# Performance work log

Hardware: AMD Instinct MI355X
Metric: run time of the kernel (lower is better)

## Reference

```python
import jax, jax.numpy as jnp
import numpy as np

H = 256  # hidden_size
B = 8192  # batch
S = 1024  # seq_length


def setup_inputs() -> dict:
    key = jax.random.key(0)
    ks = jax.random.split(key, 12)
    lim_g = 1.0 / np.sqrt(1 + H)  # torch Linear default init bound, fan_in = 1+H
    lim_o = 1.0 / np.sqrt(H)
    def lin(k, out_dim, in_dim, lim):
        kw, kb = jax.random.split(k)
        W = jax.random.uniform(kw, (out_dim, in_dim), jnp.float32, -lim, lim)
        b = jax.random.uniform(kb, (out_dim,), jnp.float32, -lim, lim)
        return W, b
    Wf, bf = lin(ks[0], H, 1 + H, lim_g)
    Wi, bi = lin(ks[1], H, 1 + H, lim_g)
    Wc, bc = lin(ks[2], H, 1 + H, lim_g)
    Wo, bo = lin(ks[3], H, 1 + H, lim_g)
    Wout, bout = lin(ks[4], 1, H, lim_o)
    x = jax.random.normal(ks[5], (B, S), jnp.float32)
    return {"x": x, "Wf": Wf, "bf": bf, "Wi": Wi, "bi": bi,
            "Wc": Wc, "bc": bc, "Wo": Wo, "bo": bo,
            "Wout": Wout, "bout": bout}


def reference(x, Wf, bf, Wi, bi, Wc, bc, Wo, bo, Wout, bout):
    B_, S_ = x.shape
    H_ = Wf.shape[0]
    # Fuse the four gate linears into one GEMM per step (same math):
    Wall = jnp.concatenate([Wf, Wi, Wc, Wo], axis=0)      # [4H, 1+H]
    ball = jnp.concatenate([bf, bi, bc, bo], axis=0)      # [4H]

    def step(carry, xt):
        h, c = carry                                       # [B,H], [B,H]
        conc = jnp.concatenate([xt[:, None], h], axis=1)   # [B, 1+H]
        g = conc @ Wall.T + ball                           # [B, 4H]
        f, i, cs, o = jnp.split(g, 4, axis=1)
        c = jax.nn.sigmoid(f) * c + jax.nn.sigmoid(i) * jnp.tanh(cs)
        h = jax.nn.sigmoid(o) * jnp.tanh(c)
        return (h, c), None

    h0 = jnp.zeros((B_, H_), x.dtype)
    c0 = jnp.zeros((B_, H_), x.dtype)
    (h, _), _ = jax.lax.scan(step, (h0, c0), x.T)          # scan over seq axis
    out = h @ Wout.T + bout                                # [B, 1]
    return out.squeeze(-1)                                 # [B]
```

## Files before the change

### kernel.cpp

```cpp
#include <hip/hip_runtime.h>
#include <hip/hip_fp16.h>


typedef _Float16 f16x8 __attribute__((ext_vector_type(8)));
typedef float f32x4 __attribute__((ext_vector_type(4)));
typedef unsigned int u32;
typedef unsigned short u16;

#define WINT_OFF 0u
#define W0B_OFF  524288u
#define FLAG_OFF 528384u
#define PUB_OFF  1048576u

static __device__ __forceinline__ float fast_exp2(float x) {
#if __has_builtin(__builtin_amdgcn_exp2f)
  return __builtin_amdgcn_exp2f(x);
#else
  return exp2f(x);
#endif
}
static __device__ __forceinline__ float fast_rcp(float x) {
#if __has_builtin(__builtin_amdgcn_rcpf)
  return __builtin_amdgcn_rcpf(x);
#else
  return 1.0f / x;
#endif
}
static __device__ __forceinline__ u16 f16b(float f) {
  union { _Float16 h; u16 u; } cv; cv.h = (_Float16)f; return cv.u;
}
static __device__ __forceinline__ float h2f(u16 u) {
  union { u16 u; _Float16 h; } cv; cv.u = u; return (float)cv.h;
}
static __device__ __forceinline__ u16* pub_base(u16* pub, int set, int par,
                                                int pid, int half) {
  return pub + ((size_t)(((set * 2 + par) * 128 + pid) * 2 + half) << 12);
}

__global__ void lstm_prep(const float* __restrict__ Wf, const float* __restrict__ Wi,
                          const float* __restrict__ Wc, const float* __restrict__ Wo,
                          const float* __restrict__ bf_, const float* __restrict__ bi_,
                          const float* __restrict__ bc_, const float* __restrict__ bo_,
                          u16* __restrict__ Wint, u32* __restrict__ w0b) {
  int n = blockIdx.x;
  int k = threadIdx.x;
  int g = n >> 8, j = n & 255;
  const float* Ws = (g == 0) ? Wf : (g == 1) ? Wi : (g == 2) ? Wc : Wo;
  const float scale = (g == 2) ? 2.88539008f : 1.44269504f;
  Wint[n * 256 + k] = f16b(Ws[j * 257 + 1 + k] * scale);
  if (k == 0) {
    const float* bs = (g == 0) ? bf_ : (g == 1) ? bi_ : (g == 2) ? bc_ : bo_;
    w0b[n] = (u32)f16b(Ws[j * 257] * scale) | ((u32)f16b(bs[j] * scale) << 16);
  }
}

__global__ void lstm_zero(uint4* __restrict__ pub4, uint4* __restrict__ flags4,
                          float* __restrict__ out, const float* __restrict__ bout) {
  int idx = blockIdx.x * 256 + threadIdx.x;
  uint4 z = uint4{0, 0, 0, 0};
  if (idx < 131072) pub4[idx] = z;
  else if (idx < 262144) pub4[idx + 131072] = z;
  else if (idx < 264192) flags4[idx - 262144] = z;
  else { int o = idx - 264192; if (o < 8192) out[o] = bout[0]; }
}

__global__ __launch_bounds__(512, 2) void lstm_main(
    const u16* __restrict__ Wint, const u32* __restrict__ w0b,
    const float* __restrict__ x, const float* __restrict__ Wout,
    float* __restrict__ out, u16* __restrict__ pub, int* __restrict__ flags) {

  __shared__ __align__(16) u16 stg[2][2][4096];

  const int tid  = threadIdx.x;
  const int wv   = tid >> 6;
  const int lane = tid & 63;
  const int l15  = lane & 15;
  const int quad = lane >> 4;
  const int B    = blockIdx.x;
  const int mi   = (B >> 3) & 1;
  const int peer = B ^ 8;
  const int pid  = (B & 7) | ((B >> 4) << 3);
  const int rows0 = pid * 64;

  f16x8 wfrag[4][8];
#pragma unroll
  for (int g = 0; g < 4; ++g)
#pragma unroll
    for (int hm = 0; hm < 2; ++hm)
#pragma unroll
      for (int ktl = 0; ktl < 4; ++ktl) {
        int kbase = (hm == 0 ? mi : 1 - mi) * 128 + ktl * 32;
        wfrag[g][hm * 4 + ktl] = *(const f16x8*)(Wint +
            (size_t)(g * 256 + mi * 128 + wv * 16 + l15) * 256 + kbase + quad * 8);
      }
  float w0f[4][4], bsf[4][4];
#pragma unroll
  for (int g = 0; g < 4; ++g) {
    uint4 wv4 = *(const uint4*)(w0b + g * 256 + mi * 128 + wv * 16 + quad * 4);
    u32 pka[4] = {wv4.x, wv4.y, wv4.z, wv4.w};
#pragma unroll
    for (int r = 0; r < 4; ++r) {
      w0f[g][r] = h2f((u16)pka[r]);
      bsf[g][r] = h2f((u16)(pka[r] >> 16));
    }
  }

#pragma unroll
  for (int i = 0; i < 4; ++i) ((uint4*)stg)[tid + i * 512] = uint4{0, 0, 0, 0};

  float cst[2][2][4];
#pragma unroll
  for (int s = 0; s < 2; ++s)
#pragma unroll
    for (int bt = 0; bt < 2; ++bt)
#pragma unroll
      for (int r = 0; r < 4; ++r) cst[s][bt][r] = 0.0f;

  const float* xq = x + (size_t)rows0 * 1024;
  float xcur[2][2];
#pragma unroll
  for (int s = 0; s < 2; ++s)
#pragma unroll
    for (int bt = 0; bt < 2; ++bt)
      xcur[s][bt] = xq[(size_t)(s * 32 + bt * 16 + l15) * 1024];

  int* const myflag = flags + B * 32;
  int* const pfl    = flags + peer * 32;

  __syncthreads();

#pragma unroll 1
  for (int t = 0; t < 1024; ++t) {
#pragma unroll
    for (int s = 0; s < 2; ++s) {
      f32x4 acc[4][2];
#pragma unroll
      for (int g = 0; g < 4; ++g)
#pragma unroll
        for (int r = 0; r < 4; ++r) {
          acc[g][0][r] = xcur[s][0] * w0f[g][r] + bsf[g][r];
          acc[g][1][r] = xcur[s][1] * w0f[g][r] + bsf[g][r];
        }
#pragma unroll
      for (int bt = 0; bt < 2; ++bt)
        xcur[s][bt] = xq[(size_t)(s * 32 + bt * 16 + l15) * 1024 + ((t + 1) & 1023)];

#pragma unroll
      for (int hm = 0; hm < 2; ++hm)
#pragma unroll
        for (int ktl = 0; ktl < 4; ++ktl) {
          f16x8 bb[2];
#pragma unroll
          for (int bt = 0; bt < 2; ++bt) {
            int b = bt * 16 + l15;
            int cp = (ktl * 4 + quad) ^ (b & 15);
            bb[bt] = *(const f16x8*)(&stg[s][hm][0] + b * 128 + cp * 8);
          }
#pragma unroll
          for (int g = 0; g < 4; ++g)
#pragma unroll
            for (int bt = 0; bt < 2; ++bt)
              acc[g][bt] = __builtin_amdgcn_mfma_f32_16x16x32_f16(
                  wfrag[g][hm * 4 + ktl], bb[bt], acc[g][bt], 0, 0, 0);
        }

      const int tn = (s == 0) ? t : t + 1;
      if (tn < 1024) {
        while (__hip_atomic_load(pfl + (s ^ 1) * 16, __ATOMIC_RELAXED,
                                 __HIP_MEMORY_SCOPE_AGENT) < tn)
          __builtin_amdgcn_s_sleep(1);
        const u16* srcO = pub_base(pub, s ^ 1, tn & 1, pid, mi);
        const u16* srcP = pub_base(pub, s ^ 1, tn & 1, pid, 1 - mi);
        __builtin_amdgcn_global_load_lds(
            (const __attribute__((address_space(1))) u32*)(srcO + wv * 512 + lane * 8),
            (__attribute__((address_space(3))) u32*)(&stg[s ^ 1][0][wv * 512]), 16, 0, 0);
        __builtin_amdgcn_global_load_lds(
            (const __attribute__((address_space(1))) u32*)(srcP + wv * 512 + lane * 8),
            (__attribute__((address_space(3))) u32*)(&stg[s ^ 1][1][wv * 512]), 16, 0, 0);
      }

      u16* pb = pub_base(pub, s, (t + 1) & 1, pid, mi);
#pragma unroll
      for (int bt = 0; bt < 2; ++bt) {
        int b = bt * 16 + l15;
        u32 lo, hi;
        {
          float h0, h1, h2, h3;
#pragma unroll
          for (int r = 0; r < 4; ++r) {
            float fg = acc[0][bt][r], ig = acc[1][bt][r];
            float cg = acc[2][bt][r], og = acc[3][bt][r];
            float Ef = fast_exp2(-fg);
            float Ei = fast_exp2(-ig);
            float C  = fast_exp2(cg);
            float X  = 1.0f + Ef;
            float Y  = (1.0f + Ei) * (C + 1.0f);
            float num = cst[s][bt][r] * Y + (C - 1.0f) * X;
            float c_  = num * fast_rcp(X * Y);
            cst[s][bt][r] = c_;
            float cc = fminf(fmaxf(c_, -40.0f), 40.0f);
            float T  = fast_exp2(2.88539008f * cc);
            float Eo = fast_exp2(-og);
            float hv = (T - 1.0f) * fast_rcp((1.0f + Eo) * (T + 1.0f));
            if (r == 0) h0 = hv; else if (r == 1) h1 = hv;
            else if (r == 2) h2 = hv; else h3 = hv;
          }
          lo = (u32)f16b(h0) | ((u32)f16b(h1) << 16);
          hi = (u32)f16b(h2) | ((u32)f16b(h3) << 16);
        }
        int c16 = wv * 2 + (quad >> 1);
        int cp  = c16 ^ (b & 15);
        *(uint2*)(pb + b * 128 + cp * 8 + (quad & 1) * 4) = uint2{lo, hi};
      }

      __syncthreads();
      if (tid == 0)
        __hip_atomic_store(myflag + s * 16, t + 1, __ATOMIC_RELAXED,
                           __HIP_MEMORY_SCOPE_AGENT);
    }
  }

  if (tid < 64) {
    int s = tid >> 5, b = tid & 31;
    const u16* pbase = pub_base(pub, s, 0, pid, mi);
    float a = 0.0f;
#pragma unroll
    for (int c = 0; c < 16; ++c) {
      f16x8 hv = *(const f16x8*)(pbase + b * 128 + ((c ^ (b & 15)) * 8));
#pragma unroll
      for (int e = 0; e < 8; ++e) a += (float)hv[e] * Wout[mi * 128 + c * 8 + e];
    }
    atomicAdd(&out[rows0 + s * 32 + b], a);
  }
}

extern "C" void kernel_launch(void* const* d_in, const int* in_sizes, int n_in,
                              void* d_out, int out_size, void* d_ws, size_t ws_size,
                              hipStream_t stream) {
  const float* x    = (const float*)d_in[0];
  const float* Wf   = (const float*)d_in[1];
  const float* bf_  = (const float*)d_in[2];
  const float* Wi   = (const float*)d_in[3];
  const float* bi_  = (const float*)d_in[4];
  const float* Wc   = (const float*)d_in[5];
  const float* bc_  = (const float*)d_in[6];
  const float* Wo   = (const float*)d_in[7];
  const float* bo_  = (const float*)d_in[8];
  const float* Wout = (const float*)d_in[9];
  const float* bout = (const float*)d_in[10];

  u16* Wint  = (u16*)((char*)d_ws + WINT_OFF);
  u32* w0b   = (u32*)((char*)d_ws + W0B_OFF);
  int* flags = (int*)((char*)d_ws + FLAG_OFF);
  u16* pub   = (u16*)((char*)d_ws + PUB_OFF);

  lstm_prep<<<1024, 256, 0, stream>>>(Wf, Wi, Wc, Wo, bf_, bi_, bc_, bo_, Wint, w0b);
  lstm_zero<<<1064, 256, 0, stream>>>((uint4*)pub, (uint4*)flags, (float*)d_out, bout);
  lstm_main<<<256, 512, 0, stream>>>(Wint, w0b, x, Wout, (float*)d_out, pub, flags);
}
```

Measured before the change: 4.664 ms.

## Software-pipeline LSTM gate epilogue with peer wait and MFMA across sub-batches

Restructures the per-step loop so the activation/cell update for the other sub-batch runs while the peer's half of h is being fetched via global_load_lds. The block's own half of h is written straight to LDS as well as to global, so only the peer half needs to be loaded. Per-step x loads replace the prefetched registers, and w0/bias are kept packed as fp16 and converted each step to save registers. Accumulators for both sub-batches stay live, which raises register pressure. A final epilogue after the loop finishes the last step.

```diff
diff --git a/kernel.cpp b/kernel.cpp
--- a/kernel.cpp
+++ b/kernel.cpp
@@ -93,17 +93,10 @@
         wfrag[g][hm * 4 + ktl] = *(const f16x8*)(Wint +
             (size_t)(g * 256 + mi * 128 + wv * 16 + l15) * 256 + kbase + quad * 8);
       }
-  float w0f[4][4], bsf[4][4];
-#pragma unroll
-  for (int g = 0; g < 4; ++g) {
-    uint4 wv4 = *(const uint4*)(w0b + g * 256 + mi * 128 + wv * 16 + quad * 4);
-    u32 pka[4] = {wv4.x, wv4.y, wv4.z, wv4.w};
-#pragma unroll
-    for (int r = 0; r < 4; ++r) {
-      w0f[g][r] = h2f((u16)pka[r]);
-      bsf[g][r] = h2f((u16)(pka[r] >> 16));
-    }
-  }
+  uint4 w0bv[4];
+#pragma unroll
+  for (int g = 0; g < 4; ++g)
+    w0bv[g] = *(const uint4*)(w0b + g * 256 + mi * 128 + wv * 16 + quad * 4);
 
 #pragma unroll
   for (int i = 0; i < 4; ++i) ((uint4*)stg)[tid + i * 512] = uint4{0, 0, 0, 0};
@@ -116,14 +109,9 @@
 #pragma unroll
       for (int r = 0; r < 4; ++r) cst[s][bt][r] = 0.0f;
 
+  f32x4 acc[2][4][2];
+
   const float* xq = x + (size_t)rows0 * 1024;
-  float xcur[2][2];
-#pragma unroll
-  for (int s = 0; s < 2; ++s)
-#pragma unroll
-    for (int bt = 0; bt < 2; ++bt)
-      xcur[s][bt] = xq[(size_t)(s * 32 + bt * 16 + l15) * 1024];
-
   int* const myflag = flags + B * 32;
   int* const pfl    = flags + peer * 32;
 
@@ -133,17 +121,74 @@
   for (int t = 0; t < 1024; ++t) {
 #pragma unroll
     for (int s = 0; s < 2; ++s) {
-      f32x4 acc[4][2];
-#pragma unroll
-      for (int g = 0; g < 4; ++g)
+      const int es  = s ^ 1;
+      const int tew = (s == 0) ? t - 1 : t;
+
+      while (__hip_atomic_load(pfl + s * 16, __ATOMIC_RELAXED,
+                               __HIP_MEMORY_SCOPE_AGENT) < t)
+        __builtin_amdgcn_s_sleep(1);
+
+      {
+        const u16* srcP = pub_base(pub, s, t & 1, pid, 1 - mi);
+        __builtin_amdgcn_global_load_lds(
+            (const __attribute__((address_space(1))) u32*)(srcP + wv * 512 + lane * 8),
+            (__attribute__((address_space(3))) u32*)(&stg[s][1][wv * 512]), 16, 0, 0);
+      }
+      __builtin_amdgcn_sched_barrier(0);
+
+      float xv0 = xq[(size_t)(s * 32 + l15) * 1024 + t];
+      float xv1 = xq[(size_t)(s * 32 + 16 + l15) * 1024 + t];
+
+      if (s == 1 || t > 0) {
+        u16* pb = pub_base(pub, es, (tew + 1) & 1, pid, mi);
+        u16* lb = &stg[es][0][0];
+#pragma unroll
+        for (int bt = 0; bt < 2; ++bt) {
+          int b = bt * 16 + l15;
+          u32 lo, hi;
+          {
+            float h0, h1, h2, h3;
+#pragma unroll
+            for (int r = 0; r < 4; ++r) {
+              float fg = acc[es][0][bt][r], ig = acc[es][1][bt][r];
+              float cg = acc[es][2][bt][r], og = acc[es][3][bt][r];
+              float Ef = fast_exp2(-fg);
+              float Ei = fast_exp2(-ig);
+              float C  = fast_exp2(cg);
+              float X  = 1.0f + Ef;
+              float Y  = (1.0f + Ei) * (C + 1.0f);
+              float num = cst[es][bt][r] * Y + (C - 1.0f) * X;
+              float c_  = num * fast_rcp(X * Y);
+              cst[es][bt][r] = c_;
+              float cc = fminf(fmaxf(c_, -40.0f), 40.0f);
+              float T  = fast_exp2(2.88539008f * cc);
+              float Eo = fast_exp2(-og);
+              float hv = (T - 1.0f) * fast_rcp((1.0f + Eo) * (T + 1.0f));
+              if (r == 0) h0 = hv; else if (r == 1) h1 = hv;
+              else if (r == 2) h2 = hv; else h3 = hv;
+            }
+            lo = (u32)f16b(h0) | ((u32)f16b(h1) << 16);
+            hi = (u32)f16b(h2) | ((u32)f16b(h3) << 16);
+          }
+          int c16 = wv * 2 + (quad >> 1);
+          int off = b * 128 + (c16 ^ (b & 15)) * 8 + (quad & 1) * 4;
+          *(uint2*)(lb + off) = uint2{lo, hi};
+          *(uint2*)(pb + off) = uint2{lo, hi};
+        }
+      }
+
+      asm volatile("s_waitcnt vmcnt(2)" ::: "memory");
+
+#pragma unroll
+      for (int g = 0; g < 4; ++g) {
+        u32 pka[4] = {w0bv[g].x, w0bv[g].y, w0bv[g].z, w0bv[g].w};
 #pragma unroll
         for (int r = 0; r < 4; ++r) {
-          acc[g][0][r] = xcur[s][0] * w0f[g][r] + bsf[g][r];
-          acc[g][1][r] = xcur[s][1] * w0f[g][r] + bsf[g][r];
-        }
-#pragma unroll
-      for (int bt = 0; bt < 2; ++bt)
-        xcur[s][bt] = xq[(size_t)(s * 32 + bt * 16 + l15) * 1024 + ((t + 1) & 1023)];
+          float w0f = h2f((u16)pka[r]), bsf = h2f((u16)(pka[r] >> 16));
+          acc[s][g][0][r] = xv0 * w0f + bsf;
+          acc[s][g][1][r] = xv1 * w0f + bsf;
+        }
+      }
 
 #pragma unroll
       for (int hm = 0; hm < 2; ++hm)
@@ -160,65 +205,52 @@
           for (int g = 0; g < 4; ++g)
 #pragma unroll
             for (int bt = 0; bt < 2; ++bt)
-              acc[g][bt] = __builtin_amdgcn_mfma_f32_16x16x32_f16(
-                  wfrag[g][hm * 4 + ktl], bb[bt], acc[g][bt], 0, 0, 0);
-        }
-
-      const int tn = (s == 0) ? t : t + 1;
-      if (tn < 1024) {
-        while (__hip_atomic_load(pfl + (s ^ 1) * 16, __ATOMIC_RELAXED,
-                                 __HIP_MEMORY_SCOPE_AGENT) < tn)
-          __builtin_amdgcn_s_sleep(1);
-        const u16* srcO = pub_base(pub, s ^ 1, tn & 1, pid, mi);
-        const u16* srcP = pub_base(pub, s ^ 1, tn & 1, pid, 1 - mi);
-        __builtin_amdgcn_global_load_lds(
-            (const __attribute__((address_space(1))) u32*)(srcO + wv * 512 + lane * 8),
-            (__attribute__((address_space(3))) u32*)(&stg[s ^ 1][0][wv * 512]), 16, 0, 0);
-        __builtin_amdgcn_global_load_lds(
-            (const __attribute__((address_space(1))) u32*)(srcP + wv * 512 + lane * 8),
-            (__attribute__((address_space(3))) u32*)(&stg[s ^ 1][1][wv * 512]), 16, 0, 0);
-      }
-
-      u16* pb = pub_base(pub, s, (t + 1) & 1, pid, mi);
-#pragma unroll
-      for (int bt = 0; bt < 2; ++bt) {
-        int b = bt * 16 + l15;
-        u32 lo, hi;
-        {
-          float h0, h1, h2, h3;
-#pragma unroll
-          for (int r = 0; r < 4; ++r) {
-            float fg = acc[0][bt][r], ig = acc[1][bt][r];
-            float cg = acc[2][bt][r], og = acc[3][bt][r];
-            float Ef = fast_exp2(-fg);
-            float Ei = fast_exp2(-ig);
-            float C  = fast_exp2(cg);
-            float X  = 1.0f + Ef;
-            float Y  = (1.0f + Ei) * (C + 1.0f);
-            float num = cst[s][bt][r] * Y + (C - 1.0f) * X;
-            float c_  = num * fast_rcp(X * Y);
-            cst[s][bt][r] = c_;
-            float cc = fminf(fmaxf(c_, -40.0f), 40.0f);
-            float T  = fast_exp2(2.88539008f * cc);
-            float Eo = fast_exp2(-og);
-            float hv = (T - 1.0f) * fast_rcp((1.0f + Eo) * (T + 1.0f));
-            if (r == 0) h0 = hv; else if (r == 1) h1 = hv;
-            else if (r == 2) h2 = hv; else h3 = hv;
-          }
-          lo = (u32)f16b(h0) | ((u32)f16b(h1) << 16);
-          hi = (u32)f16b(h2) | ((u32)f16b(h3) << 16);
-        }
-        int c16 = wv * 2 + (quad >> 1);
-        int cp  = c16 ^ (b & 15);
-        *(uint2*)(pb + b * 128 + cp * 8 + (quad & 1) * 4) = uint2{lo, hi};
-      }
+              acc[s][g][bt] = __builtin_amdgcn_mfma_f32_16x16x32_f16(
+                  wfrag[g][hm * 4 + ktl], bb[bt], acc[s][g][bt], 0, 0, 0);
+        }
 
       __syncthreads();
       if (tid == 0)
-        __hip_atomic_store(myflag + s * 16, t + 1, __ATOMIC_RELAXED,
+        __hip_atomic_store(myflag + es * 16, tew + 1, __ATOMIC_RELAXED,
                            __HIP_MEMORY_SCOPE_AGENT);
     }
   }
+
+  {
+    u16* pb = pub_base(pub, 1, 0, pid, mi);
+#pragma unroll
+    for (int bt = 0; bt < 2; ++bt) {
+      int b = bt * 16 + l15;
+      u32 lo, hi;
+      {
+        float h0, h1, h2, h3;
+#pragma unroll
+        for (int r = 0; r < 4; ++r) {
+          float fg = acc[1][0][bt][r], ig = acc[1][1][bt][r];
+          float cg = acc[1][2][bt][r], og = acc[1][3][bt][r];
+          float Ef = fast_exp2(-fg);
+          float Ei = fast_exp2(-ig);
+          float C  = fast_exp2(cg);
+          float X  = 1.0f + Ef;
+          float Y  = (1.0f + Ei) * (C + 1.0f);
+          float num = cst[1][bt][r] * Y + (C - 1.0f) * X;
+          float c_  = num * fast_rcp(X * Y);
+          float cc = fminf(fmaxf(c_, -40.0f), 40.0f);
+          float T  = fast_exp2(2.88539008f * cc);
+          float Eo = fast_exp2(-og);
+          float hv = (T - 1.0f) * fast_rcp((1.0f + Eo) * (T + 1.0f));
+          if (r == 0) h0 = hv; else if (r == 1) h1 = hv;
+          else if (r == 2) h2 = hv; else h3 = hv;
+        }
+        lo = (u32)f16b(h0) | ((u32)f16b(h1) << 16);
+        hi = (u32)f16b(h2) | ((u32)f16b(h3) << 16);
+      }
+      int c16 = wv * 2 + (quad >> 1);
+      int off = b * 128 + (c16 ^ (b & 15)) * 8 + (quad & 1) * 4;
+      *(uint2*)(pb + off) = uint2{lo, hi};
+    }
+  }
+  __syncthreads();
 
   if (tid < 64) {
     int s = tid >> 5, b = tid & 31;
```

Result: slower. 5.255 ms (+12.7%).
